# Optimization experiments

Measured on AMD Instinct MI355X. Metric: run time of the kernel, lower is better.

The kernel has to match this reference:

```python
import jax, jax.numpy as jnp
import numpy as np

KS = 7
DIM = 1024
HEADS = 16
B = 2048

def _rpb_index(ks):
    # Replicates the torch buffer: relative_position_index, shape [ks*ks, ks*ks]
    ch = np.arange(ks)
    coords = np.stack(np.meshgrid(ch, ch, indexing='ij')).reshape(2, -1)  # [2, N]
    rel = coords[:, :, None] - coords[:, None, :]                          # [2, N, N]
    rel = rel.transpose(1, 2, 0).copy()                                    # [N, N, 2]
    rel[:, :, 0] += ks - 1
    rel[:, :, 1] += ks - 1
    rel[:, :, 0] *= 2 * ks - 1
    idx = np.flipud(np.fliplr(rel.sum(-1)))
    return jnp.asarray(idx.copy())

def setup_inputs() -> dict:
    key = jax.random.key(0)
    ks = jax.random.split(key, 4)
    x = jax.random.normal(ks[0], (B, KS, KS, DIM), dtype=jnp.float32)
    qkv_w = jax.random.normal(ks[1], (3 * DIM, DIM), dtype=jnp.float32) * (DIM ** -0.5)
    qkv_b = jnp.zeros((3 * DIM,), dtype=jnp.float32)
    rpb = jax.random.normal(ks[2], (HEADS, 2 * KS - 1, 2 * KS - 1), dtype=jnp.float32) * 0.02
    proj_w = jax.random.normal(ks[3], (DIM, DIM), dtype=jnp.float32) * (DIM ** -0.5)
    proj_b = jnp.zeros((DIM,), dtype=jnp.float32)
    return {"x": x, "qkv_w": qkv_w, "qkv_b": qkv_b, "rpb": rpb, "proj_w": proj_w, "proj_b": proj_b}

def reference(x, qkv_w, qkv_b, rpb, proj_w, proj_b):
    Bn, H, W, C = x.shape
    ksz = H
    N = H * W
    heads = rpb.shape[0]
    hd = C // heads
    scale = hd ** -0.5
    idx = _rpb_index(ksz)  # [N, N] int

    qkv = x.reshape(Bn, N, C) @ qkv_w.T + qkv_b              # [B, N, 3C]
    qkv = qkv.reshape(Bn, N, 3, heads, hd).transpose(2, 0, 3, 1, 4)  # [3, B, h, N, hd]
    q, k, v = qkv[0] * scale, qkv[1], qkv[2]

    attn = jnp.einsum('bhnd,bhmd->bhnm', q, k)               # [B, h, N, N]
    # gather relative-position bias: rpb[h, 2k-1, 2k-1] -> flat [(2k-1)^2, h] -> [N, N, h]
    bias = rpb.transpose(1, 2, 0).reshape(-1, heads)[idx.reshape(-1)]
    bias = bias.reshape(N, N, heads).transpose(2, 0, 1)      # [h, N, N]
    attn = jax.nn.softmax(attn + bias[None], axis=-1)

    out = jnp.einsum('bhnm,bhmd->bhnd', attn, v)             # [B, h, N, hd]
    out = out.transpose(0, 2, 1, 3).reshape(Bn, H, W, C)
    return out @ proj_w.T + proj_b
```

## Files before the change

kernel.cpp:

```cpp
#include <hip/hip_runtime.h>


typedef _Float16 f16;
typedef _Float16 f16x8 __attribute__((ext_vector_type(8)));
typedef _Float16 f16x4 __attribute__((ext_vector_type(4)));
typedef float f32x4 __attribute__((ext_vector_type(4)));

#define G1P(p) ((const __attribute__((address_space(1))) unsigned int*)(p))
#define L3P(p) ((__attribute__((address_space(3))) unsigned int*)(p))

static const size_t MROW_MAX = 100351;

__global__ void cvt_kernel(const float* __restrict__ in, f16* __restrict__ out, int n4) {
  int i = blockIdx.x * blockDim.x + threadIdx.x;
  int stride = gridDim.x * blockDim.x;
  const float4* in4 = (const float4*)in;
  f16x4* out4 = (f16x4*)out;
  for (; i < n4; i += stride) {
    float4 v = in4[i];
    f16x4 o = { (f16)v.x, (f16)v.y, (f16)v.z, (f16)v.w };
    out4[i] = o;
  }
}

__global__ void bias_kernel(const float* __restrict__ rpb, float* __restrict__ bias_t) {
  int h = blockIdx.x;
  for (int e = threadIdx.x; e < 4096; e += blockDim.x) {
    int m = e >> 6, n = e & 63;
    float v = -1e30f;
    if (n < 49 && m < 49) {
      int in_ = n / 7, jn = n % 7, im = m / 7, jm = m % 7;
      v = rpb[h * 169 + (im - in_ + 6) * 13 + (jm - jn + 6)];
    }
    bias_t[h * 4096 + e] = v * 1.44269504f;
  }
}

#define VM4 asm volatile("s_waitcnt vmcnt(4)" ::: "memory")
#define VM0 asm volatile("s_waitcnt vmcnt(0)" ::: "memory")
#define NOVM ((void)0)
#define NOSTG ((void)0)

#define STAGE(GB, ROW0, COL0, LDSOFF)                                              \
  {                                                                                \
    const f16* s0_ = (GB) + (size_t)((ROW0) + wid * 32 + srow) * K + ((COL0) + sce); \
    __builtin_amdgcn_global_load_lds(G1P(s0_), L3P(lds + (LDSOFF) + wid * 2048), 16, 0, 0); \
    const f16* s1_ = s0_ + (size_t)16 * K;                                         \
    __builtin_amdgcn_global_load_lds(G1P(s1_), L3P(lds + (LDSOFF) + wid * 2048 + 1024), 16, 0, 0); \
  }

#define MFMA4(AREG, ROW)                                                           \
  acc[ROW][0] = __builtin_amdgcn_mfma_f32_16x16x32_f16(AREG, b0, acc[ROW][0], 0, 0, 0); \
  acc[ROW][1] = __builtin_amdgcn_mfma_f32_16x16x32_f16(AREG, b1, acc[ROW][1], 0, 0, 0); \
  acc[ROW][2] = __builtin_amdgcn_mfma_f32_16x16x32_f16(AREG, b2, acc[ROW][2], 0, 0, 0); \
  acc[ROW][3] = __builtin_amdgcn_mfma_f32_16x16x32_f16(AREG, b3, acc[ROW][3], 0, 0, 0);

#define PHASE(ABASE, BBASE, MH, STG, VMW)                                          \
  {                                                                                \
    f16x8 a0 = *(const f16x8*)((ABASE) + (wm * 128 + (MH) * 64 +  0 + l15) * 64 + swz); \
    f16x8 a1 = *(const f16x8*)((ABASE) + (wm * 128 + (MH) * 64 + 16 + l15) * 64 + swz); \
    f16x8 a2 = *(const f16x8*)((ABASE) + (wm * 128 + (MH) * 64 + 32 + l15) * 64 + swz); \
    f16x8 a3 = *(const f16x8*)((ABASE) + (wm * 128 + (MH) * 64 + 48 + l15) * 64 + swz); \
    if ((MH) == 0) {                                                               \
      b0 = *(const f16x8*)((BBASE) + (wn * 64 +  0 + l15) * 64 + swz);             \
      b1 = *(const f16x8*)((BBASE) + (wn * 64 + 16 + l15) * 64 + swz);             \
      b2 = *(const f16x8*)((BBASE) + (wn * 64 + 32 + l15) * 64 + swz);             \
      b3 = *(const f16x8*)((BBASE) + (wn * 64 + 48 + l15) * 64 + swz);             \
    }                                                                              \
    STG;                                                                           \
    __builtin_amdgcn_s_barrier();                                                  \
    asm volatile("s_waitcnt lgkmcnt(0)" ::: "memory");                             \
    __builtin_amdgcn_sched_barrier(0);                                             \
    __builtin_amdgcn_s_setprio(1);                                                 \
    MFMA4(a0, (MH) * 4 + 0) MFMA4(a1, (MH) * 4 + 1)                                \
    MFMA4(a2, (MH) * 4 + 2) MFMA4(a3, (MH) * 4 + 3)                                \
    __builtin_amdgcn_s_setprio(0);                                                 \
    VMW;                                                                           \
    __builtin_amdgcn_s_barrier();                                                  \
  }

template <typename OutT>
__global__ __launch_bounds__(512, 2)
void gemm256(const f16* __restrict__ A, const f16* __restrict__ B,
             const float* __restrict__ bias, OutT* __restrict__ C,
             int N, int K, int ntiles_n) {
  __shared__ char lds[131072];
  const int tid = threadIdx.x;
  const int wid = tid >> 6, ln = tid & 63;
  const int l15 = ln & 15, lhi = ln >> 4;
  const int wm = wid >> 2, wn = wid & 3;
  const int srow = ln >> 2;
  const int sce = (((ln & 3) ^ ((ln >> 3) & 3)) << 3);
  const int swz = ((lhi ^ ((l15 >> 1) & 3)) << 4);

  const int nblk = gridDim.x;
  const int wg = (blockIdx.x & 7) * (nblk >> 3) + (blockIdx.x >> 3);
  const int bn = wg % ntiles_n, bm = wg / ntiles_n;
  const int m0 = bm * 256, n0 = bn * 256;

  f32x4 acc[8][4];
#pragma unroll
  for (int i = 0; i < 8; ++i)
#pragma unroll
    for (int j = 0; j < 4; ++j) acc[i][j] = (f32x4){0.f, 0.f, 0.f, 0.f};
  f16x8 b0, b1, b2, b3;

  STAGE(A, m0, 0, 0);
  STAGE(B, n0, 0, 32768);
  STAGE(A, m0, 32, 16384);
  STAGE(B, n0, 32, 49152);
  STAGE(A, m0, 64, 65536);
  STAGE(B, n0, 64, 98304);
  VM4;
  __builtin_amdgcn_s_barrier();

  for (int i = 0; i < 7; ++i) {
    const int cT1k1 = (2 * i + 1) * 64 + 32;
    const int cT2k0 = (2 * i + 2) * 64;
    const int cT2k1 = cT2k0 + 32;
    const int cT3k0 = (2 * i + 3) * 64;
    PHASE(lds + 0,      lds + 32768,  0, STAGE(A, m0, cT1k1, 81920),  NOVM);
    PHASE(lds + 0,      lds + 32768,  1, STAGE(B, n0, cT1k1, 114688), NOVM);
    PHASE(lds + 16384,  lds + 49152,  0, STAGE(A, m0, cT2k0, 0),      NOVM);
    PHASE(lds + 16384,  lds + 49152,  1, STAGE(B, n0, cT2k0, 32768),  VM4);
    PHASE(lds + 65536,  lds + 98304,  0, STAGE(A, m0, cT2k1, 16384),  NOVM);
    PHASE(lds + 65536,  lds + 98304,  1, STAGE(B, n0, cT2k1, 49152),  NOVM);
    PHASE(lds + 81920,  lds + 114688, 0, STAGE(A, m0, cT3k0, 65536),  NOVM);
    PHASE(lds + 81920,  lds + 114688, 1, STAGE(B, n0, cT3k0, 98304),  VM4);
  }
  PHASE(lds + 0,      lds + 32768,  0, STAGE(A, m0, 15 * 64 + 32, 81920),  NOVM);
  PHASE(lds + 0,      lds + 32768,  1, STAGE(B, n0, 15 * 64 + 32, 114688), NOVM);
  PHASE(lds + 16384,  lds + 49152,  0, NOSTG, NOVM);
  PHASE(lds + 16384,  lds + 49152,  1, NOSTG, VM0);
  PHASE(lds + 65536,  lds + 98304,  0, NOSTG, NOVM);
  PHASE(lds + 65536,  lds + 98304,  1, NOSTG, NOVM);
  PHASE(lds + 81920,  lds + 114688, 0, NOSTG, NOVM);
  PHASE(lds + 81920,  lds + 114688, 1, NOSTG, NOVM);

  float bv[4];
#pragma unroll
  for (int j = 0; j < 4; ++j) bv[j] = bias[n0 + wn * 64 + j * 16 + l15];
#pragma unroll
  for (int ii = 0; ii < 8; ++ii)
#pragma unroll
    for (int j = 0; j < 4; ++j)
#pragma unroll
      for (int r = 0; r < 4; ++r) {
        int gr = m0 + wm * 128 + ii * 16 + lhi * 4 + r;
        int gc = n0 + wn * 64 + j * 16 + l15;
        C[(size_t)gr * N + gc] = (OutT)(acc[ii][j][r] + bv[j]);
      }
}

__global__ __launch_bounds__(128, 4)
void attn_kernel(const f16* __restrict__ qkv,
                 const float* __restrict__ bias_t,
                 f16* __restrict__ out) {
  __shared__ char lds[16384];
  const int bh = blockIdx.x;
  const int b = bh >> 4, h = bh & 15;
  const int tid = threadIdx.x;
  const int w = tid >> 6;
  const int ln = tid & 63;
  const int l15 = ln & 15, lhi = ln >> 4;
  const size_t base = (size_t)b * 49;
  const int nbase = w * 32;

  f16x8 qf[2][2];
#pragma unroll
  for (int t = 0; t < 2; ++t) {
    size_t row = base + nbase + t * 16 + l15;
    if (row > MROW_MAX) row = MROW_MAX;
    const f16* qp = qkv + row * 3072 + h * 64 + lhi * 8;
    qf[t][0] = *(const f16x8*)(qp);
    qf[t][1] = *(const f16x8*)(qp + 32);
  }

  {
    size_t row = base + ln;
    if (row > MROW_MAX) row = MROW_MAX;
    const f16* vp = qkv + row * 3072 + 2048 + h * 64 + nbase;
    f16x8 vr[4];
#pragma unroll
    for (int j = 0; j < 4; ++j) vr[j] = *(const f16x8*)(vp + j * 8);
#pragma unroll
    for (int dd = 0; dd < 32; ++dd) {
      int d = nbase + dd;
      *(f16*)(lds + 8192 + d * 128 + ((ln * 2) ^ ((d & 7) << 4))) = vr[dd >> 3][dd & 7];
    }
  }

  f32x4 acc[2][4];
#pragma unroll
  for (int i = 0; i < 2; ++i)
#pragma unroll
    for (int j = 0; j < 4; ++j) acc[i][j] = (f32x4){0.f, 0.f, 0.f, 0.f};
#pragma unroll
  for (int kk = 0; kk < 2; ++kk) {
    f16x8 bf[4];
#pragma unroll
    for (int t = 0; t < 4; ++t) {
      size_t row = base + t * 16 + l15;
      if (row > MROW_MAX) row = MROW_MAX;
      bf[t] = *(const f16x8*)(qkv + row * 3072 + 1024 + h * 64 + kk * 32 + lhi * 8);
    }
#pragma unroll
    for (int i = 0; i < 2; ++i)
#pragma unroll
      for (int j = 0; j < 4; ++j)
        acc[i][j] = __builtin_amdgcn_mfma_f32_16x16x32_f16(qf[i][kk], bf[j], acc[i][j], 0, 0, 0);
  }

  __syncthreads();

  const float SC = 0.125f * 1.44269504f;
  const float* bb = bias_t + h * 4096;
#pragma unroll
  for (int i = 0; i < 2; ++i) {
    float4 bq[4];
#pragma unroll
    for (int j = 0; j < 4; ++j)
      bq[j] = *(const float4*)(bb + (j * 16 + l15) * 64 + nbase + i * 16 + lhi * 4);
#pragma unroll
    for (int r = 0; r < 4; ++r) {
      int n = nbase + i * 16 + lhi * 4 + r;
      float lv[4];
#pragma unroll
      for (int j = 0; j < 4; ++j)
        lv[j] = acc[i][j][r] * SC + ((const float*)&bq[j])[r];
      float Mx = fmaxf(fmaxf(lv[0], lv[1]), fmaxf(lv[2], lv[3]));
#pragma unroll
      for (int off = 1; off < 16; off <<= 1) Mx = fmaxf(Mx, __shfl_xor(Mx, off));
      float s = 0.f;
#pragma unroll
      for (int j = 0; j < 4; ++j) { lv[j] = exp2f(lv[j] - Mx); s += lv[j]; }
#pragma unroll
      for (int off = 1; off < 16; off <<= 1) s += __shfl_xor(s, off);
      float inv = 1.f / s;
#pragma unroll
      for (int j = 0; j < 4; ++j) {
        int m = j * 16 + l15;
        *(f16*)(lds + n * 128 + ((m * 2) ^ ((n & 7) << 4))) = (f16)(lv[j] * inv);
      }
    }
  }

  f32x4 o[2][4];
#pragma unroll
  for (int i = 0; i < 2; ++i)
#pragma unroll
    for (int j = 0; j < 4; ++j) o[i][j] = (f32x4){0.f, 0.f, 0.f, 0.f};
#pragma unroll
  for (int kk = 0; kk < 2; ++kk) {
    f16x8 af[2], bf[4];
#pragma unroll
    for (int t = 0; t < 2; ++t) {
      int nr = nbase + t * 16 + l15;
      af[t] = *(const f16x8*)(lds + nr * 128 + ((kk * 64 + lhi * 16) ^ ((nr & 7) << 4)));
    }
#pragma unroll
    for (int u = 0; u < 4; ++u) {
      int dr = u * 16 + l15;
      bf[u] = *(const f16x8*)(lds + 8192 + dr * 128 + ((kk * 64 + lhi * 16) ^ ((dr & 7) << 4)));
    }
#pragma unroll
    for (int i = 0; i < 2; ++i)
#pragma unroll
      for (int j = 0; j < 4; ++j)
        o[i][j] = __builtin_amdgcn_mfma_f32_16x16x32_f16(af[i], bf[j], o[i][j], 0, 0, 0);
  }
#pragma unroll
  for (int i = 0; i < 2; ++i)
#pragma unroll
    for (int j = 0; j < 4; ++j)
#pragma unroll
      for (int r = 0; r < 4; ++r) {
        int n = nbase + i * 16 + lhi * 4 + r;
        if (n < 49)
          out[(base + n) * 1024 + h * 64 + j * 16 + l15] = (f16)o[i][j][r];
      }
}

extern "C" void kernel_launch(void* const* d_in, const int* in_sizes, int n_in,
                              void* d_out, int out_size, void* d_ws, size_t ws_size,
                              hipStream_t stream) {
  const float* x      = (const float*)d_in[0];
  const float* qkv_w  = (const float*)d_in[1];
  const float* qkv_b  = (const float*)d_in[2];
  const float* rpb    = (const float*)d_in[3];
  const float* proj_w = (const float*)d_in[4];
  const float* proj_b = (const float*)d_in[5];
  float* out = (float*)d_out;

  char* ws = (char*)d_ws;
  f16*   x16      = (f16*)(ws);
  f16*   wq16     = (f16*)(ws + 205520896);
  f16*   wp16     = (f16*)(ws + 211812352);
  f16*   qkv16    = (f16*)(ws + 213909504);
  f16*   attn16   = (f16*)(ws + 830472192);
  float* bias_t   = (float*)(ws + 1035993088);

  cvt_kernel<<<2048, 256, 0, stream>>>(x, x16, 102760448 / 4);
  cvt_kernel<<<1024, 256, 0, stream>>>(qkv_w, wq16, 3145728 / 4);
  cvt_kernel<<<512, 256, 0, stream>>>(proj_w, wp16, 1048576 / 4);
  bias_kernel<<<16, 64, 0, stream>>>(rpb, bias_t);

  gemm256<f16><<<4704, 512, 0, stream>>>(x16, wq16, qkv_b, qkv16, 3072, 1024, 12);
  attn_kernel<<<2048 * 16, 128, 0, stream>>>(qkv16, bias_t, attn16);
  gemm256<float><<<1568, 512, 0, stream>>>(attn16, wp16, proj_b, out, 1024, 1024, 4);
}
```

Measured before the change: 1.384 ms.

## Split attention across four waves and stage K in LDS via direct loads

The attention block grows from two to four waves, and each wave now handles 16 query rows instead of 32. K is loaded once per block into swizzled LDS with global_load_lds. Before, every wave fetched the full K tile from global memory into registers. The V transpose is also spread across all four waves. This cuts redundant global K traffic and register pressure per wave and raises parallelism, at the cost of an extra block barrier and a dependence on the asynchronous LDS loads finishing before that barrier.

```diff
diff --git a/kernel.cpp b/kernel.cpp
--- a/kernel.cpp
+++ b/kernel.cpp
@@ -152,7 +152,7 @@
       }
 }
 
-__global__ __launch_bounds__(128, 4)
+__global__ __launch_bounds__(256, 4)
 void attn_kernel(const f16* __restrict__ qkv,
                  const float* __restrict__ bias_t,
                  f16* __restrict__ out) {
@@ -164,70 +164,80 @@
   const int ln = tid & 63;
   const int l15 = ln & 15, lhi = ln >> 4;
   const size_t base = (size_t)b * 49;
-  const int nbase = w * 32;
-
-  f16x8 qf[2][2];
-#pragma unroll
-  for (int t = 0; t < 2; ++t) {
-    size_t row = base + nbase + t * 16 + l15;
+  const int nbase = w * 16;
+
+  {
+    int rA = ln >> 3, lc = ln & 7;
+#pragma unroll
+    for (int cc = 0; cc < 2; ++cc) {
+      int c = w * 2 + cc;
+      int r = c * 8 + rA;
+      int ce = (lc ^ (r & 7)) << 3;
+      size_t row = base + r;
+      if (row > MROW_MAX) row = MROW_MAX;
+      const f16* g = qkv + row * 3072 + 1024 + h * 64 + ce;
+      __builtin_amdgcn_global_load_lds(G1P(g), L3P(lds + c * 1024), 16, 0, 0);
+    }
+  }
+
+  f16x8 qf[2];
+  {
+    size_t row = base + nbase + l15;
     if (row > MROW_MAX) row = MROW_MAX;
     const f16* qp = qkv + row * 3072 + h * 64 + lhi * 8;
-    qf[t][0] = *(const f16x8*)(qp);
-    qf[t][1] = *(const f16x8*)(qp + 32);
+    qf[0] = *(const f16x8*)(qp);
+    qf[1] = *(const f16x8*)(qp + 32);
   }
 
   {
     size_t row = base + ln;
     if (row > MROW_MAX) row = MROW_MAX;
     const f16* vp = qkv + row * 3072 + 2048 + h * 64 + nbase;
-    f16x8 vr[4];
-#pragma unroll
-    for (int j = 0; j < 4; ++j) vr[j] = *(const f16x8*)(vp + j * 8);
-#pragma unroll
-    for (int dd = 0; dd < 32; ++dd) {
+    f16x8 vr[2];
+    vr[0] = *(const f16x8*)(vp);
+    vr[1] = *(const f16x8*)(vp + 8);
+#pragma unroll
+    for (int dd = 0; dd < 16; ++dd) {
       int d = nbase + dd;
       *(f16*)(lds + 8192 + d * 128 + ((ln * 2) ^ ((d & 7) << 4))) = vr[dd >> 3][dd & 7];
     }
   }
 
-  f32x4 acc[2][4];
-#pragma unroll
-  for (int i = 0; i < 2; ++i)
-#pragma unroll
-    for (int j = 0; j < 4; ++j) acc[i][j] = (f32x4){0.f, 0.f, 0.f, 0.f};
+  __syncthreads();
+
+  f32x4 acc[4];
+#pragma unroll
+  for (int j = 0; j < 4; ++j) acc[j] = (f32x4){0.f, 0.f, 0.f, 0.f};
 #pragma unroll
   for (int kk = 0; kk < 2; ++kk) {
     f16x8 bf[4];
 #pragma unroll
     for (int t = 0; t < 4; ++t) {
-      size_t row = base + t * 16 + l15;
-      if (row > MROW_MAX) row = MROW_MAX;
-      bf[t] = *(const f16x8*)(qkv + row * 3072 + 1024 + h * 64 + kk * 32 + lhi * 8);
-    }
-#pragma unroll
-    for (int i = 0; i < 2; ++i)
-#pragma unroll
-      for (int j = 0; j < 4; ++j)
-        acc[i][j] = __builtin_amdgcn_mfma_f32_16x16x32_f16(qf[i][kk], bf[j], acc[i][j], 0, 0, 0);
+      int mr = t * 16 + l15;
+      int pb = (kk * 64 + lhi * 16) ^ ((mr & 7) << 4);
+      bf[t] = *(const f16x8*)(lds + mr * 128 + pb);
+    }
+#pragma unroll
+    for (int j = 0; j < 4; ++j)
+      acc[j] = __builtin_amdgcn_mfma_f32_16x16x32_f16(qf[kk], bf[j], acc[j], 0, 0, 0);
   }
 
   __syncthreads();
 
   const float SC = 0.125f * 1.44269504f;
   const float* bb = bias_t + h * 4096;
-#pragma unroll
-  for (int i = 0; i < 2; ++i) {
+  {
     float4 bq[4];
 #pragma unroll
     for (int j = 0; j < 4; ++j)
-      bq[j] = *(const float4*)(bb + (j * 16 + l15) * 64 + nbase + i * 16 + lhi * 4);
+      bq[j] = *(const float4*)(bb + (j * 16 + l15) * 64 + nbase + lhi * 4);
 #pragma unroll
     for (int r = 0; r < 4; ++r) {
-      int n = nbase + i * 16 + lhi * 4 + r;
+      int n = nbase + lhi * 4 + r;
       float lv[4];
 #pragma unroll
       for (int j = 0; j < 4; ++j)
-        lv[j] = acc[i][j][r] * SC + ((const float*)&bq[j])[r];
+        lv[j] = acc[j][r] * SC + ((const float*)&bq[j])[r];
       float Mx = fmaxf(fmaxf(lv[0], lv[1]), fmaxf(lv[2], lv[3]));
 #pragma unroll
       for (int off = 1; off < 16; off <<= 1) Mx = fmaxf(Mx, __shfl_xor(Mx, off));
@@ -245,18 +255,15 @@
     }
   }
 
-  f32x4 o[2][4];
-#pragma unroll
-  for (int i = 0; i < 2; ++i)
-#pragma unroll
-    for (int j = 0; j < 4; ++j) o[i][j] = (f32x4){0.f, 0.f, 0.f, 0.f};
+  f32x4 o[4];
+#pragma unroll
+  for (int j = 0; j < 4; ++j) o[j] = (f32x4){0.f, 0.f, 0.f, 0.f};
 #pragma unroll
   for (int kk = 0; kk < 2; ++kk) {
-    f16x8 af[2], bf[4];
-#pragma unroll
-    for (int t = 0; t < 2; ++t) {
-      int nr = nbase + t * 16 + l15;
-      af[t] = *(const f16x8*)(lds + nr * 128 + ((kk * 64 + lhi * 16) ^ ((nr & 7) << 4)));
+    f16x8 af, bf[4];
+    {
+      int nr = nbase + l15;
+      af = *(const f16x8*)(lds + nr * 128 + ((kk * 64 + lhi * 16) ^ ((nr & 7) << 4)));
     }
 #pragma unroll
     for (int u = 0; u < 4; ++u) {
@@ -264,21 +271,17 @@
       bf[u] = *(const f16x8*)(lds + 8192 + dr * 128 + ((kk * 64 + lhi * 16) ^ ((dr & 7) << 4)));
     }
 #pragma unroll
-    for (int i = 0; i < 2; ++i)
-#pragma unroll
-      for (int j = 0; j < 4; ++j)
-        o[i][j] = __builtin_amdgcn_mfma_f32_16x16x32_f16(af[i], bf[j], o[i][j], 0, 0, 0);
-  }
-#pragma unroll
-  for (int i = 0; i < 2; ++i)
-#pragma unroll
     for (int j = 0; j < 4; ++j)
-#pragma unroll
-      for (int r = 0; r < 4; ++r) {
-        int n = nbase + i * 16 + lhi * 4 + r;
-        if (n < 49)
-          out[(base + n) * 1024 + h * 64 + j * 16 + l15] = (f16)o[i][j][r];
-      }
+      o[j] = __builtin_amdgcn_mfma_f32_16x16x32_f16(af, bf[j], o[j], 0, 0, 0);
+  }
+#pragma unroll
+  for (int j = 0; j < 4; ++j)
+#pragma unroll
+    for (int r = 0; r < 4; ++r) {
+      int n = nbase + lhi * 4 + r;
+      if (n < 49)
+        out[(base + n) * 1024 + h * 64 + j * 16 + l15] = (f16)o[j][r];
+    }
 }
 
 extern "C" void kernel_launch(void* const* d_in, const int* in_sizes, int n_in,
@@ -306,6 +309,6 @@
   bias_kernel<<<16, 64, 0, stream>>>(rpb, bias_t);
 
   gemm256<f16><<<4704, 512, 0, stream>>>(x16, wq16, qkv_b, qkv16, 3072, 1024, 12);
-  attn_kernel<<<2048 * 16, 128, 0, stream>>>(qkv16, bias_t, attn16);
+  attn_kernel<<<2048 * 16, 256, 0, stream>>>(qkv16, bias_t, attn16);
   gemm256<float><<<1568, 512, 0, stream>>>(attn16, wp16, proj_b, out, 1024, 1024, 4);
 }
```

After: 1.383 ms. No clear change (-0.1%).
